# Optimization experiments

Hardware: AMD Instinct MI355X
Metric: run time of the kernel (lower is better)

The kernel has to match this reference:

```python
import jax, jax.numpy as jnp
import numpy as np

B, T, C, H = 4, 2048, 1024, 16
D = C // H  # head_dim = 64


def setup_inputs() -> dict:
    key = jax.random.key(0)
    k1, k2, k3 = jax.random.split(key, 3)
    x = jax.random.normal(k1, (B, T, C), dtype=jnp.float32)
    # torch Linear init ~ U(-1/sqrt(fan_in), 1/sqrt(fan_in)); scaled normal is fine for a baseline
    w_qkv = jax.random.normal(k2, (C, 3 * C), dtype=jnp.float32) * (1.0 / np.sqrt(C))
    w_proj = jax.random.normal(k3, (C, C), dtype=jnp.float32) * (1.0 / np.sqrt(C))
    return {"x": x, "w_qkv": w_qkv, "w_proj": w_proj}


def reference(x, w_qkv, w_proj):
    Bb, Tt, Cc = x.shape
    qkv = x @ w_qkv                                   # [B,T,3C]
    q, k, v = jnp.split(qkv, 3, axis=-1)
    # [B,T,C] -> [B,H,T,D]
    q = q.reshape(Bb, Tt, H, D).transpose(0, 2, 1, 3)
    k = k.reshape(Bb, Tt, H, D).transpose(0, 2, 1, 3)
    v = v.reshape(Bb, Tt, H, D).transpose(0, 2, 1, 3)
    scale = 1.0 / np.sqrt(D).astype(np.float32)
    logits = jnp.einsum("bhqd,bhkd->bhqk", q, k) * scale  # [B,H,T,T]
    causal = jnp.tril(jnp.ones((Tt, Tt), dtype=bool))
    logits = jnp.where(causal, logits, jnp.finfo(logits.dtype).min)
    attn = jax.nn.softmax(logits, axis=-1)
    y = jnp.einsum("bhqk,bhkd->bhqd", attn, v)            # [B,H,T,D]
    y = y.transpose(0, 2, 1, 3).reshape(Bb, Tt, Cc)
    return y @ w_proj                                     # dropout p=0 (eval)
```

## Files before the change

kernel.cpp:

```cpp
#include <hip/hip_runtime.h>
#include <hip/hip_bf16.h>
#include <stdint.h>

typedef unsigned short u16;
typedef __attribute__((ext_vector_type(4))) float f32x4;
typedef __attribute__((ext_vector_type(16))) float f32x16;
typedef __attribute__((ext_vector_type(8))) __bf16 bf16x8;
typedef __attribute__((ext_vector_type(2))) unsigned int u32x2;

__device__ __forceinline__ u16 f2bf(float f) {
  union { float f; uint32_t u; } x; x.f = f;
  const uint32_t u = x.u;
  return (u16)((u + 0x7fffu + ((u >> 16) & 1u)) >> 16);
}

#define QSCALE 0.1803368801111244f

__global__ void cvt_f32_bf16(const float* __restrict__ in, u16* __restrict__ out,
                             int n) {
  const int i = (blockIdx.x * blockDim.x + threadIdx.x) * 4;
  if (i < n) {
    const float4 v = *(const float4*)(in + i);
    ushort4 o;
    o.x = f2bf(v.x); o.y = f2bf(v.y); o.z = f2bf(v.z); o.w = f2bf(v.w);
    *(ushort4*)(out + i) = o;
  }
}

__global__ void transpose_cvt(const float* __restrict__ in, u16* __restrict__ out,
                              int R, int Cc) {
  __shared__ u16 tile[64][66];
  const int tx = threadIdx.x, ty = threadIdx.y;
  const int c0 = blockIdx.x * 64, r0 = blockIdx.y * 64;
#pragma unroll
  for (int i = 0; i < 4; ++i)
    tile[ty + i * 16][tx] = f2bf(in[(size_t)(r0 + ty + i * 16) * Cc + c0 + tx]);
  __syncthreads();
#pragma unroll
  for (int i = 0; i < 4; ++i)
    out[(size_t)(c0 + ty + i * 16) * R + r0 + tx] = tile[tx][ty + i * 16];
}

__global__ void transpose_v(const u16* __restrict__ V, u16* __restrict__ VT) {
  __shared__ u16 tile[64][66];
  const int tx = threadIdx.x, ty = threadIdx.y;
  const int r0 = blockIdx.x * 64;
  const size_t ho = (size_t)blockIdx.y * 2048 * 64;
  const u16* in = V + ho;
  u16* out = VT + ho;
#pragma unroll
  for (int i = 0; i < 4; ++i)
    tile[ty + i * 16][tx] = in[(size_t)(r0 + ty + i * 16) * 64 + tx];
  __syncthreads();
#pragma unroll
  for (int i = 0; i < 4; ++i)
    out[(size_t)(ty + i * 16) * 2048 + r0 + tx] = tile[tx][ty + i * 16];
}

template <int MODE>
__global__ __launch_bounds__(256) void gemm_bt(
    const u16* __restrict__ A, const u16* __restrict__ BT,
    float* __restrict__ out, u16* __restrict__ Qo, u16* __restrict__ Ko,
    u16* __restrict__ Vo, int M, int N, int K) {
  __shared__ u16 Asm_[128 * 32];
  __shared__ u16 Bsm_[128 * 32];
  const int tid = threadIdx.x;
  const int wid = tid >> 6, lane = tid & 63;
  const int wm = wid >> 1, wn = wid & 1;
  const int l15 = lane & 15, l4 = lane >> 4;
  const int bm = blockIdx.y, bn = blockIdx.x;

  const u16* Ag = A + (size_t)bm * 128 * K;
  const u16* Bg = BT + (size_t)bn * 128 * K;

  f32x4 acc[4][4] = {};

  const int srow = lane >> 2;
  const int scol = (lane & 3) * 8;

  for (int kt = 0; kt < K; kt += 32) {
    __syncthreads();
#pragma unroll
    for (int it = 0; it < 2; ++it) {
      const int c = it * 4 + wid;
      const int row = c * 16 + srow;
      __builtin_amdgcn_global_load_lds(
          (const __attribute__((address_space(1))) uint32_t*)(Ag + (size_t)row * K + kt + scol),
          (__attribute__((address_space(3))) uint32_t*)(&Asm_[c * 512]), 16, 0, 0);
      __builtin_amdgcn_global_load_lds(
          (const __attribute__((address_space(1))) uint32_t*)(Bg + (size_t)row * K + kt + scol),
          (__attribute__((address_space(3))) uint32_t*)(&Bsm_[c * 512]), 16, 0, 0);
    }
    __syncthreads();

    bf16x8 af[4], bfr[4];
#pragma unroll
    for (int m = 0; m < 4; ++m)
      af[m] = *(const bf16x8*)&Asm_[(wm * 64 + m * 16 + l15) * 32 + l4 * 8];
#pragma unroll
    for (int n = 0; n < 4; ++n)
      bfr[n] = *(const bf16x8*)&Bsm_[(wn * 64 + n * 16 + l15) * 32 + l4 * 8];
#pragma unroll
    for (int m = 0; m < 4; ++m)
#pragma unroll
      for (int n = 0; n < 4; ++n)
        acc[m][n] = __builtin_amdgcn_mfma_f32_16x16x32_bf16(af[m], bfr[n], acc[m][n], 0, 0, 0);
  }

  const int row0 = bm * 128 + wm * 64;
  const int col0 = bn * 128 + wn * 64;
#pragma unroll
  for (int m = 0; m < 4; ++m) {
#pragma unroll
    for (int n = 0; n < 4; ++n) {
#pragma unroll
      for (int j = 0; j < 4; ++j) {
        const int row = row0 + m * 16 + l4 * 4 + j;
        const int col = col0 + n * 16 + l15;
        if (MODE == 1) {
          const int sec = col >> 10, c = col & 1023;
          const int h = c >> 6, d = c & 63;
          const int b = row >> 11, t = row & 2047;
          float av = acc[m][n][j];
          if (sec == 0) av *= QSCALE;
          u16* dst = (sec == 0) ? Qo : (sec == 1) ? Ko : Vo;
          dst[(((size_t)(b * 16 + h)) * 2048 + t) * 64 + d] = f2bf(av);
        } else {
          out[(size_t)row * N + col] = acc[m][n][j];
        }
      }
    }
  }
}

__global__ __launch_bounds__(256, 4) void attn_fwd(const u16* __restrict__ Qp,
                                                   const u16* __restrict__ Kp,
                                                   const u16* __restrict__ VTp,
                                                   u16* __restrict__ Y) {
  constexpr int DP = 72;
  constexpr float THR = 11.0f;
  __shared__ u16 Ks[64 * DP];
  __shared__ u16 Vt[64 * DP];

  const int xorm = (int)((0x0A050F00u >> ((blockIdx.y >> 4) * 8)) & 15u);
  const int qt = (int)blockIdx.x ^ xorm;
  const int bh = blockIdx.y;
  const int b = bh >> 4, h = bh & 15;
  const int tid = threadIdx.x, wid = tid >> 6, lane = tid & 63;
  const int l31 = lane & 31, hb = lane >> 5;

  const size_t head_off = (size_t)bh * 2048 * 64;
  const u16* Kh = Kp + head_off;
  const u16* VTh = VTp + head_off;

  const int qg = qt * 128 + wid * 32 + l31;
  const u16* Qrow = Qp + head_off + (size_t)qg * 64;

  bf16x8 qf[4];
#pragma unroll
  for (int d = 0; d < 4; ++d)
    qf[d] = *(const bf16x8*)(Qrow + d * 16 + hb * 8);

  float m_ = -1e30f, l_ = 0.f;
  f32x16 oacc[2] = {};

  const int nt = 2 * qt + 2;
  for (int kt = 0; kt < nt; ++kt) {
    __syncthreads();
#pragma unroll
    for (int it = 0; it < 2; ++it) {
      const int idx = it * 256 + tid;
      const int r = idx >> 3;
      const int c = (idx & 7) * 8;
      *(bf16x8*)&Ks[r * DP + c] = *(const bf16x8*)(Kh + (size_t)(kt * 64 + r) * 64 + c);
      *(bf16x8*)&Vt[r * DP + c] = *(const bf16x8*)(VTh + (size_t)r * 2048 + kt * 64 + c);
    }
    __syncthreads();

    const bool diag = (kt >= 2 * qt);

#pragma unroll
    for (int kb2 = 0; kb2 < 2; ++kb2) {
      f32x16 s = {};
      __builtin_amdgcn_s_setprio(1);
#pragma unroll
      for (int d = 0; d < 4; ++d) {
        const bf16x8 kf = *(const bf16x8*)&Ks[(kb2 * 32 + l31) * DP + d * 16 + hb * 8];
        s = __builtin_amdgcn_mfma_f32_32x32x16_bf16(kf, qf[d], s, 0, 0, 0);
      }
      __builtin_amdgcn_s_setprio(0);

      if (diag) {
        const int kbase = kt * 64 + kb2 * 32 + hb * 4;
#pragma unroll
        for (int r = 0; r < 16; ++r) {
          const int koff = (r & 3) + 8 * (r >> 2);
          if (kbase + koff > qg) s[r] = -1e30f;
        }
      }

      float pmax = s[0];
#pragma unroll
      for (int r = 1; r < 16; ++r) pmax = fmaxf(pmax, s[r]);
      if (!__all(pmax - m_ <= THR)) {
        const float fm = fmaxf(pmax, __shfl_xor(pmax, 32));
        const float mnew = fmaxf(m_, fm);
        const float alpha = __builtin_exp2f(m_ - mnew);
        m_ = mnew;
        l_ *= alpha;
#pragma unroll
        for (int nb = 0; nb < 2; ++nb)
#pragma unroll
          for (int r = 0; r < 16; ++r) oacc[nb][r] *= alpha;
      }
#pragma unroll
      for (int r = 0; r < 16; ++r) {
        s[r] = __builtin_exp2f(s[r] - m_);
        l_ += s[r];
      }

      bf16x8 pb[2];
#pragma unroll
      for (int st = 0; st < 2; ++st) {
        uint32_t x0, x1, y0, y1;
        asm("v_cvt_pk_bf16_f32 %0, %1, %2" : "=v"(x0) : "v"(s[8 * st + 0]), "v"(s[8 * st + 1]));
        asm("v_cvt_pk_bf16_f32 %0, %1, %2" : "=v"(x1) : "v"(s[8 * st + 2]), "v"(s[8 * st + 3]));
        asm("v_cvt_pk_bf16_f32 %0, %1, %2" : "=v"(y0) : "v"(s[8 * st + 4]), "v"(s[8 * st + 5]));
        asm("v_cvt_pk_bf16_f32 %0, %1, %2" : "=v"(y1) : "v"(s[8 * st + 6]), "v"(s[8 * st + 7]));
        const u32x2 r0 = __builtin_amdgcn_permlane32_swap(x0, y0, false, false);
        const u32x2 r1 = __builtin_amdgcn_permlane32_swap(x1, y1, false, false);
        union { uint32_t w[4]; bf16x8 v; } u;
        u.w[0] = r0[0]; u.w[1] = r1[0]; u.w[2] = r0[1]; u.w[3] = r1[1];
        pb[st] = u.v;
      }

      __builtin_amdgcn_s_setprio(1);
#pragma unroll
      for (int nb = 0; nb < 2; ++nb)
#pragma unroll
        for (int st = 0; st < 2; ++st) {
          const bf16x8 vf = *(const bf16x8*)&Vt[(nb * 32 + l31) * DP + kb2 * 32 + st * 16 + hb * 8];
          oacc[nb] = __builtin_amdgcn_mfma_f32_32x32x16_bf16(vf, pb[st], oacc[nb], 0, 0, 0);
        }
      __builtin_amdgcn_s_setprio(0);
    }
  }

  const float lf = l_ + __shfl_xor(l_, 32);
  const float inv = 1.0f / lf;
  u16* Yrow = Y + ((size_t)b * 2048 + qg) * 1024 + h * 64;
#pragma unroll
  for (int nb = 0; nb < 2; ++nb) {
#pragma unroll
    for (int g = 0; g < 4; ++g) {
      ushort4 o;
      o.x = f2bf(oacc[nb][4 * g + 0] * inv);
      o.y = f2bf(oacc[nb][4 * g + 1] * inv);
      o.z = f2bf(oacc[nb][4 * g + 2] * inv);
      o.w = f2bf(oacc[nb][4 * g + 3] * inv);
      *(ushort4*)(Yrow + nb * 32 + g * 8 + hb * 4) = o;
    }
  }
}

extern "C" void kernel_launch(void* const* d_in, const int* in_sizes, int n_in,
                              void* d_out, int out_size, void* d_ws,
                              size_t ws_size, hipStream_t stream) {
  const float* x = (const float*)d_in[0];
  const float* w_qkv = (const float*)d_in[1];
  const float* w_proj = (const float*)d_in[2];
  float* out = (float*)d_out;

  char* ws = (char*)d_ws;
  u16* xb = (u16*)ws;
  u16* VTw = (u16*)ws;
  u16* wqkvT = (u16*)(ws + 16777216);
  u16* wprojT = (u16*)(ws + 23068672);
  u16* Qw = (u16*)(ws + 25165824);
  u16* Kw = (u16*)(ws + 41943040);
  u16* Vw = (u16*)(ws + 58720256);
  u16* Yw = (u16*)(ws + 75497472);
  if (ws_size < 92274688) return;

  cvt_f32_bf16<<<dim3(8192), dim3(256), 0, stream>>>(x, xb, 8388608);

  dim3 tb(64, 16);
  transpose_cvt<<<dim3(48, 16), tb, 0, stream>>>(w_qkv, wqkvT, 1024, 3072);
  transpose_cvt<<<dim3(16, 16), tb, 0, stream>>>(w_proj, wprojT, 1024, 1024);

  gemm_bt<1><<<dim3(24, 64), dim3(256), 0, stream>>>(
      xb, wqkvT, (float*)nullptr, Qw, Kw, Vw, 8192, 3072, 1024);

  transpose_v<<<dim3(32, 64), tb, 0, stream>>>(Vw, VTw);

  attn_fwd<<<dim3(16, 64), dim3(256), 0, stream>>>(Qw, Kw, VTw, Yw);

  gemm_bt<0><<<dim3(8, 64), dim3(256), 0, stream>>>(
      Yw, wprojT, out, (u16*)nullptr, (u16*)nullptr, (u16*)nullptr,
      8192, 1024, 1024);
}
```

Baseline: 203.5 us.

## Double-buffer K/V tiles in attention with register prefetch of next tile

The attention kernel now issues the global loads for the next K and V tile into registers before computing on the current tile, then writes them into a second LDS buffer after compute. This overlaps global memory latency with MFMA work and cuts the two barriers per iteration to one. In exchange it doubles LDS use (about 36KB per block) and adds register pressure, which may lower occupancy under launch_bounds(256,4).

```diff
diff --git a/kernel.cpp b/kernel.cpp
--- a/kernel.cpp
+++ b/kernel.cpp
@@ -139,14 +139,15 @@
                                                    u16* __restrict__ Y) {
   constexpr int DP = 72;
   constexpr float THR = 11.0f;
-  __shared__ u16 Ks[64 * DP];
-  __shared__ u16 Vt[64 * DP];
+  __shared__ u16 Ks[2][64 * DP];
+  __shared__ u16 Vt[2][64 * DP];
 
   const int xorm = (int)((0x0A050F00u >> ((blockIdx.y >> 4) * 8)) & 15u);
   const int qt = (int)blockIdx.x ^ xorm;
   const int bh = blockIdx.y;
   const int b = bh >> 4, h = bh & 15;
-  const int tid = threadIdx.x, wid = tid >> 6, lane = tid & 63;
+  const int tid = threadIdx.x, lane = tid & 63;
+  const int wid = tid >> 6;
   const int l31 = lane & 31, hb = lane >> 5;
 
   const size_t head_off = (size_t)bh * 2048 * 64;
@@ -164,18 +165,36 @@
   float m_ = -1e30f, l_ = 0.f;
   f32x16 oacc[2] = {};
 
+  const int sr = tid >> 3;
+  const int sc = (tid & 7) * 8;
+
+  bf16x8 kreg[2], vreg[2];
+  auto kvload = [&](int kt) {
+#pragma unroll
+    for (int it = 0; it < 2; ++it) {
+      const int r = sr + it * 32;
+      kreg[it] = *(const bf16x8*)(Kh + (size_t)(kt * 64 + r) * 64 + sc);
+      vreg[it] = *(const bf16x8*)(VTh + (size_t)r * 2048 + kt * 64 + sc);
+    }
+  };
+  auto kvwrite = [&](int buf) {
+#pragma unroll
+    for (int it = 0; it < 2; ++it) {
+      const int r = sr + it * 32;
+      *(bf16x8*)&Ks[buf][r * DP + sc] = kreg[it];
+      *(bf16x8*)&Vt[buf][r * DP + sc] = vreg[it];
+    }
+  };
+
+  kvload(0);
+  kvwrite(0);
+  __syncthreads();
+
   const int nt = 2 * qt + 2;
   for (int kt = 0; kt < nt; ++kt) {
-    __syncthreads();
-#pragma unroll
-    for (int it = 0; it < 2; ++it) {
-      const int idx = it * 256 + tid;
-      const int r = idx >> 3;
-      const int c = (idx & 7) * 8;
-      *(bf16x8*)&Ks[r * DP + c] = *(const bf16x8*)(Kh + (size_t)(kt * 64 + r) * 64 + c);
-      *(bf16x8*)&Vt[r * DP + c] = *(const bf16x8*)(VTh + (size_t)r * 2048 + kt * 64 + c);
-    }
-    __syncthreads();
+    const int cur = kt & 1;
+    const bool havenext = (kt + 1 < nt);
+    if (havenext) kvload(kt + 1);
 
     const bool diag = (kt >= 2 * qt);
 
@@ -185,7 +204,7 @@
       __builtin_amdgcn_s_setprio(1);
 #pragma unroll
       for (int d = 0; d < 4; ++d) {
-        const bf16x8 kf = *(const bf16x8*)&Ks[(kb2 * 32 + l31) * DP + d * 16 + hb * 8];
+        const bf16x8 kf = *(const bf16x8*)&Ks[cur][(kb2 * 32 + l31) * DP + d * 16 + hb * 8];
         s = __builtin_amdgcn_mfma_f32_32x32x16_bf16(kf, qf[d], s, 0, 0, 0);
       }
       __builtin_amdgcn_s_setprio(0);
@@ -239,11 +258,14 @@
       for (int nb = 0; nb < 2; ++nb)
 #pragma unroll
         for (int st = 0; st < 2; ++st) {
-          const bf16x8 vf = *(const bf16x8*)&Vt[(nb * 32 + l31) * DP + kb2 * 32 + st * 16 + hb * 8];
+          const bf16x8 vf = *(const bf16x8*)&Vt[cur][(nb * 32 + l31) * DP + kb2 * 32 + st * 16 + hb * 8];
           oacc[nb] = __builtin_amdgcn_mfma_f32_32x32x16_bf16(vf, pb[st], oacc[nb], 0, 0, 0);
         }
       __builtin_amdgcn_s_setprio(0);
     }
+
+    if (havenext) kvwrite(cur ^ 1);
+    __syncthreads();
   }
 
   const float lf = l_ + __shfl_xor(l_, 32);
```

Result: no change. 203.2 us (-0.1%).
